# Kernel tuning notes

Hardware: AMD Instinct MI355X
Metric: run time of the kernel (lower is better)

The kernel has to match this reference:

```python
import jax, jax.numpy as jnp
import numpy as np

NEG_INF = -9e15
ALPHA = 0.2  # LeakyReLU negative slope

N = 8192
D_IN = 512
D_OUT = 256


def setup_inputs() -> dict:
    key = jax.random.key(0)
    k1, k2, k3, k4, k5 = jax.random.split(key, 5)
    features = jax.random.normal(k1, (N, D_IN), dtype=jnp.float32)
    adjacency_matrix = jax.random.randint(k2, (N, N), 0, 2, dtype=jnp.int32)
    # learned params (torch Linear stores [out, in]; we use [in, out] layout)
    s_phi = 1.0 / np.sqrt(D_IN)
    W_phi = jax.random.uniform(k3, (D_IN, D_OUT), jnp.float32, -s_phi, s_phi)
    s_v = 1.0 / np.sqrt(D_OUT)
    w_mu = jax.random.uniform(k4, (D_OUT,), jnp.float32, -s_v, s_v)
    w_xi = jax.random.uniform(k5, (D_OUT,), jnp.float32, -s_v, s_v)
    return {"features": features, "adjacency_matrix": adjacency_matrix,
            "W_phi": W_phi, "w_mu": w_mu, "w_xi": w_xi}


def reference(features, adjacency_matrix, W_phi, w_mu, w_xi):
    h = features @ W_phi                                   # [N, d_out]
    mu = h @ w_mu                                          # [N]
    xi = h @ w_xi                                          # [N]
    e = mu[:, None] + xi[None, :]                          # [N, N] additive scores
    e = jnp.where(e >= 0, e, ALPHA * e)                    # LeakyReLU
    e = jnp.where(adjacency_matrix > 0, e, NEG_INF)        # mask non-edges
    a = jax.nn.softmax(e, axis=1)                          # row softmax (dropout p=0)
    out = a @ h                                            # weighted aggregation
    return jax.nn.elu(out)
```

## Files before the change

kernel.cpp:

```cpp
#include <hip/hip_runtime.h>
#include <cstdint>
#include <cstddef>


#define LOG2E 1.44269504f

typedef __attribute__((ext_vector_type(8))) short short8;
typedef __attribute__((ext_vector_type(4))) float floatx4;

using uint_as1 = __attribute__((address_space(1))) unsigned int;
using uint_as3 = __attribute__((address_space(3))) unsigned int;

__device__ __forceinline__ void gld_lds16(const void* g, void* l) {
  __builtin_amdgcn_global_load_lds((const uint_as1*)g, (uint_as3*)l, 16, 0, 0);
}

__device__ __forceinline__ unsigned short f2b(float f) {
  unsigned u = __float_as_uint(f);
  u += 0x7fffu + ((u >> 16) & 1u);
  return (unsigned short)(u >> 16);
}
__device__ __forceinline__ float b2f(short s) {
  return __uint_as_float(((unsigned)(unsigned short)s) << 16);
}

__device__ __forceinline__ unsigned cvtpk_bf16(float a, float b) {
  unsigned r;
  asm("v_cvt_pk_bf16_f32 %0, %1, %2" : "=v"(r) : "v"(a), "v"(b));
  return r;
}

__global__ void k_bitmaskz(const int* __restrict__ adj,
                           const float* __restrict__ Emu, const float* __restrict__ Fmu,
                           const float* __restrict__ Exi, const float* __restrict__ Fxi,
                           unsigned long long* __restrict__ bm, float* __restrict__ zbuf) {
  int gw = (blockIdx.x * 256 + threadIdx.x) >> 6;
  int lane = threadIdx.x & 63;
  float EM = Emu[gw], FM = Fmu[gw];
  size_t w0 = (size_t)gw * 128;
  float z = 0.f;
  for (int r = 0; r < 128; r += 4) {
    size_t wd = w0 + r;
    int v0 = adj[(wd + 0) * 64 + lane];
    int v1 = adj[(wd + 1) * 64 + lane];
    int v2 = adj[(wd + 2) * 64 + lane];
    int v3 = adj[(wd + 3) * 64 + lane];
    float e0 = Exi[(r + 0) * 64 + lane], f0 = Fxi[(r + 0) * 64 + lane];
    float e1 = Exi[(r + 1) * 64 + lane], f1 = Fxi[(r + 1) * 64 + lane];
    float e2 = Exi[(r + 2) * 64 + lane], f2 = Fxi[(r + 2) * 64 + lane];
    float e3 = Exi[(r + 3) * 64 + lane], f3 = Fxi[(r + 3) * 64 + lane];
    unsigned long long m0 = __ballot(v0 != 0);
    unsigned long long m1 = __ballot(v1 != 0);
    unsigned long long m2 = __ballot(v2 != 0);
    unsigned long long m3 = __ballot(v3 != 0);
    z += (v0 != 0) ? fmaxf(EM * e0, FM * f0) : 0.f;
    z += (v1 != 0) ? fmaxf(EM * e1, FM * f1) : 0.f;
    z += (v2 != 0) ? fmaxf(EM * e2, FM * f2) : 0.f;
    z += (v3 != 0) ? fmaxf(EM * e3, FM * f3) : 0.f;
    if (lane == 0) {
      bm[wd] = m0; bm[wd + 1] = m1; bm[wd + 2] = m2; bm[wd + 3] = m3;
    }
  }
#pragma unroll
  for (int off = 32; off > 0; off >>= 1) z += __shfl_xor(z, off);
  if (lane == 0) zbuf[gw] = z;
}

__global__ void k_cvt_features(const float* __restrict__ f, unsigned short* __restrict__ fb) {
  int tid = blockIdx.x * 256 + threadIdx.x;
  float4 v = ((const float4*)f)[tid];
  ushort4 o = {f2b(v.x), f2b(v.y), f2b(v.z), f2b(v.w)};
  *(ushort4*)&fb[tid * 4] = o;
}

__global__ void k_prep_wt(const float* __restrict__ w, unsigned short* __restrict__ wt) {
  int tid = blockIdx.x * 256 + threadIdx.x;
  int n = tid >> 9, k = tid & 511;
  wt[n * 512 + k] = f2b(w[k * 256 + n]);
}

__global__ void k_prep_p(const float* __restrict__ w, const float* __restrict__ wmu,
                         const float* __restrict__ wxi, float* __restrict__ pmu,
                         float* __restrict__ pxi) {
  int tid = blockIdx.x * 256 + threadIdx.x;
  int k = tid >> 2, seg = tid & 3;
  float sm = 0.f, sx = 0.f;
  int base = k * 256 + seg * 64;
#pragma unroll
  for (int c = 0; c < 64; c += 4) {
    float4 wv = *(const float4*)&w[base + c];
    float4 mv = *(const float4*)&wmu[seg * 64 + c];
    float4 xv = *(const float4*)&wxi[seg * 64 + c];
    sm += wv.x * mv.x + wv.y * mv.y + wv.z * mv.z + wv.w * mv.w;
    sx += wv.x * xv.x + wv.y * xv.y + wv.z * xv.z + wv.w * xv.w;
  }
  sm += __shfl_xor(sm, 1); sm += __shfl_xor(sm, 2);
  sx += __shfl_xor(sx, 1); sx += __shfl_xor(sx, 2);
  if (seg == 0) { pmu[k] = sm; pxi[k] = sx; }
}

__global__ void k_mu_xi(const unsigned short* __restrict__ fb, const float* __restrict__ pmu,
                        const float* __restrict__ pxi, float* __restrict__ Emu,
                        float* __restrict__ Fmu, float* __restrict__ Exi,
                        float* __restrict__ Fxi) {
  int w = threadIdx.x >> 6, l = threadIdx.x & 63;
  int i = blockIdx.x * 4 + w;
  short8 fv = *(const short8*)&fb[i * 512 + l * 8];
  float m = 0.f, x = 0.f;
#pragma unroll
  for (int c = 0; c < 8; ++c) {
    float fvf = b2f(fv[c]);
    m = fmaf(fvf, pmu[l * 8 + c], m);
    x = fmaf(fvf, pxi[l * 8 + c], x);
  }
#pragma unroll
  for (int off = 32; off > 0; off >>= 1) {
    m += __shfl_xor(m, off);
    x += __shfl_xor(x, off);
  }
  if (l == 0) {
    float ms = m * LOG2E, xs = x * LOG2E;
    Emu[i] = __builtin_amdgcn_exp2f(ms);
    Fmu[i] = __builtin_amdgcn_exp2f(0.2f * ms);
    Exi[i] = __builtin_amdgcn_exp2f(xs);
    Fxi[i] = __builtin_amdgcn_exp2f(0.2f * xs);
  }
}

__global__ __launch_bounds__(256, 2) void k_gemm1(const unsigned short* __restrict__ fb,
                                                  const unsigned short* __restrict__ wt,
                                                  unsigned short* __restrict__ ht) {
  __shared__ __align__(16) unsigned short As[64 * 64];
  __shared__ __align__(16) unsigned short Bs[128 * 64];
  int t = threadIdx.x, w = t >> 6, l = t & 63;
  int bm_ = blockIdx.x >> 1, bn = blockIdx.x & 1;
  int m0 = bm_ * 64, n0 = bn * 128;
  int lr = l >> 3, lg = l & 7, g = lg ^ lr;
  int kg = l >> 4, ln = l & 15;
  floatx4 zero = {0.f, 0.f, 0.f, 0.f};
  floatx4 acc[4][2];
#pragma unroll
  for (int mf = 0; mf < 4; ++mf)
#pragma unroll
    for (int nf = 0; nf < 2; ++nf) acc[mf][nf] = zero;

  for (int it = 0; it < 8; ++it) {
    int k0 = it * 64;
#pragma unroll
    for (int q = 0; q < 2; ++q) {
      int row = w * 16 + q * 8 + lr;
      const void* gp = fb + (size_t)(m0 + row) * 512 + k0 + g * 8;
      int lb = __builtin_amdgcn_readfirstlane((w * 16 + q * 8) * 64);
      gld_lds16(gp, &As[lb]);
    }
#pragma unroll
    for (int q = 0; q < 4; ++q) {
      int row = w * 32 + q * 8 + lr;
      const void* gp = wt + (size_t)(n0 + row) * 512 + k0 + g * 8;
      int lb = __builtin_amdgcn_readfirstlane((w * 32 + q * 8) * 64);
      gld_lds16(gp, &Bs[lb]);
    }
    __syncthreads();
#pragma unroll
    for (int ks = 0; ks < 2; ++ks) {
      int gg = ks * 4 + kg;
      int swz = (gg ^ (ln & 7)) * 8;
      short8 bfr[2];
#pragma unroll
      for (int nf = 0; nf < 2; ++nf)
        bfr[nf] = *(const short8*)&Bs[(w * 32 + nf * 16 + ln) * 64 + swz];
#pragma unroll
      for (int mf = 0; mf < 4; ++mf) {
        short8 afr = *(const short8*)&As[(mf * 16 + ln) * 64 + swz];
#pragma unroll
        for (int nf = 0; nf < 2; ++nf)
          acc[mf][nf] = __builtin_amdgcn_mfma_f32_16x16x32_bf16(afr, bfr[nf], acc[mf][nf], 0, 0, 0);
      }
    }
    __syncthreads();
  }
#pragma unroll
  for (int mf = 0; mf < 4; ++mf)
#pragma unroll
    for (int nf = 0; nf < 2; ++nf) {
      int ng = n0 + w * 32 + nf * 16 + ln;
      int mg = m0 + mf * 16 + kg * 4;
      ushort4 o = {f2b(acc[mf][nf][0]), f2b(acc[mf][nf][1]),
                   f2b(acc[mf][nf][2]), f2b(acc[mf][nf][3])};
      *(ushort4*)&ht[(size_t)ng * 8192 + mg] = o;
    }
}

__global__ __launch_bounds__(512, 2) void k_gatt8(const unsigned char* __restrict__ bm8,
                                                  const unsigned short* __restrict__ ht,
                                                  const float* __restrict__ Emu,
                                                  const float* __restrict__ Fmu,
                                                  const float* __restrict__ Exi,
                                                  const float* __restrict__ Fxi,
                                                  float* __restrict__ nump) {
  __shared__ __align__(16) unsigned short Bs[2][256 * 128];
  __shared__ __align__(16) float EfE[1024];
  __shared__ __align__(16) float EfF[1024];

  int t = threadIdx.x, w = t >> 6, l = t & 63;
  int ln = l & 15, kg = l >> 4;
  int jb = blockIdx.x & 7, ig = blockIdx.x >> 3;
  int i0 = ig * 256;
  int jc0 = jb * 1024;

  if (t < 256) {
    *(float4*)&EfE[t * 4] = *(const float4*)&Exi[jc0 + t * 4];
  } else {
    int t2 = t - 256;
    *(float4*)&EfF[t2 * 4] = *(const float4*)&Fxi[jc0 + t2 * 4];
  }

  float EM[2], FM[2];
  const uint4* bprow[2];
#pragma unroll
  for (int mf = 0; mf < 2; ++mf) {
    int i = i0 + w * 32 + mf * 16 + ln;
    EM[mf] = Emu[i];
    FM[mf] = Fmu[i];
    bprow[mf] = (const uint4*)(bm8 + (size_t)i * 1024 + jb * 128);
  }

  floatx4 zero = {0.f, 0.f, 0.f, 0.f};
  floatx4 acc[2][16];
#pragma unroll
  for (int mf = 0; mf < 2; ++mf)
#pragma unroll
    for (int nf = 0; nf < 16; ++nf) acc[mf][nf] = zero;

#define STAGE(win_, b_)                                                       \
  {                                                                           \
    int j0_ = jc0 + (win_) * 128;                                             \
    _Pragma("unroll")                                                         \
    for (int q = 0; q < 8; ++q) {                                             \
      int r0 = w * 32 + q * 4;                                                \
      int row = r0 + (l >> 4);                                                \
      int g = (l & 15) ^ (row & 15);                                          \
      const void* gp = ht + (size_t)row * 8192 + j0_ + g * 8;                 \
      int lb = __builtin_amdgcn_readfirstlane((b_) * (256 * 128) + r0 * 128); \
      gld_lds16(gp, &Bs[0][lb]);                                              \
    }                                                                         \
  }

  uint4 bc[2], bnx[2];
#pragma unroll
  for (int mf = 0; mf < 2; ++mf) bc[mf] = bprow[mf][0];
  STAGE(0, 0);
  __syncthreads();

  for (int win = 0; win < 8; ++win) {
    int buf = win & 1;
    if (win < 7) {
      STAGE(win + 1, buf ^ 1);
#pragma unroll
      for (int mf = 0; mf < 2; ++mf) bnx[mf] = bprow[mf][win + 1];
    }
#pragma unroll
    for (int ksl = 0; ksl < 4; ++ksl) {
      int gran = ksl * 4 + kg;
      int jl = win * 128 + gran * 8;
      float4 e0 = *(const float4*)&EfE[jl];
      float4 e1 = *(const float4*)&EfE[jl + 4];
      float4 f0 = *(const float4*)&EfF[jl];
      float4 f1 = *(const float4*)&EfF[jl + 4];
      float ex[8] = {e0.x, e0.y, e0.z, e0.w, e1.x, e1.y, e1.z, e1.w};
      float fx[8] = {f0.x, f0.y, f0.z, f0.w, f1.x, f1.y, f1.z, f1.w};
      short8 af[2];
#pragma unroll
      for (int mf = 0; mf < 2; ++mf) {
        unsigned word = (ksl == 0) ? bc[mf].x : (ksl == 1) ? bc[mf].y
                      : (ksl == 2) ? bc[mf].z : bc[mf].w;
        unsigned bits = (word >> (kg * 8)) & 0xffu;
        float A = EM[mf], F = FM[mf];
        union { unsigned u[4]; short8 s; } cv;
#pragma unroll
        for (int p = 0; p < 4; ++p) {
          float m0 = fmaxf(A * ex[2 * p], F * fx[2 * p]);
          float m1 = fmaxf(A * ex[2 * p + 1], F * fx[2 * p + 1]);
          m0 = (bits & (1u << (2 * p))) ? m0 : 0.f;
          m1 = (bits & (1u << (2 * p + 1))) ? m1 : 0.f;
          cv.u[p] = cvtpk_bf16(m0, m1);
        }
        af[mf] = cv.s;
      }
#pragma unroll
      for (int half = 0; half < 2; ++half) {
        short8 bfv[8];
#pragma unroll
        for (int nf = 0; nf < 8; ++nf) {
          int n = half * 128 + nf * 16 + ln;
          bfv[nf] = *(const short8*)&Bs[buf][n * 128 + ((gran ^ (n & 15)) * 8)];
        }
#pragma unroll
        for (int mf = 0; mf < 2; ++mf)
#pragma unroll
          for (int nf = 0; nf < 8; ++nf)
            acc[mf][half * 8 + nf] = __builtin_amdgcn_mfma_f32_16x16x32_bf16(
                af[mf], bfv[nf], acc[mf][half * 8 + nf], 0, 0, 0);
      }
    }
    __syncthreads();
#pragma unroll
    for (int mf = 0; mf < 2; ++mf) bc[mf] = bnx[mf];
  }
#undef STAGE

  float* np = nump + (size_t)jb * (8192 * 256);
#pragma unroll
  for (int mf = 0; mf < 2; ++mf) {
    int rowb = i0 + w * 32 + mf * 16 + kg * 4;
#pragma unroll
    for (int r = 0; r < 4; ++r) {
      float* rp = np + (size_t)(rowb + r) * 256;
#pragma unroll
      for (int nf = 0; nf < 16; ++nf)
        rp[nf * 16 + ln] = acc[mf][nf][r];
    }
  }
}

__global__ void k_final(const float* __restrict__ nump, const float* __restrict__ zbuf,
                        float* __restrict__ out) {
  int tid = blockIdx.x * 256 + threadIdx.x;
  int i = tid >> 6;
  float zi = 1.0f / zbuf[i];
  float4 v = {0.f, 0.f, 0.f, 0.f};
#pragma unroll
  for (int p = 0; p < 8; ++p) {
    float4 s = *(const float4*)&nump[(size_t)p * (8192 * 256) + tid * 4];
    v.x += s.x; v.y += s.y; v.z += s.z; v.w += s.w;
  }
  v.x *= zi; v.y *= zi; v.z *= zi; v.w *= zi;
  v.x = (v.x > 0.f) ? v.x : (__builtin_amdgcn_exp2f(v.x * LOG2E) - 1.f);
  v.y = (v.y > 0.f) ? v.y : (__builtin_amdgcn_exp2f(v.y * LOG2E) - 1.f);
  v.z = (v.z > 0.f) ? v.z : (__builtin_amdgcn_exp2f(v.z * LOG2E) - 1.f);
  v.w = (v.w > 0.f) ? v.w : (__builtin_amdgcn_exp2f(v.w * LOG2E) - 1.f);
  *(float4*)&out[tid * 4] = v;
}

extern "C" void kernel_launch(void* const* d_in, const int* in_sizes, int n_in,
                              void* d_out, int out_size, void* d_ws, size_t ws_size,
                              hipStream_t stream) {
  const float* features = (const float*)d_in[0];
  const int* adjm = (const int*)d_in[1];
  const float* W_phi = (const float*)d_in[2];
  const float* w_mu = (const float*)d_in[3];
  const float* w_xi = (const float*)d_in[4];
  float* out = (float*)d_out;

  char* ws = (char*)d_ws;
  unsigned short* fb  = (unsigned short*)(ws + 0);
  unsigned short* ht  = (unsigned short*)(ws + 8388608);
  unsigned short* wt  = (unsigned short*)(ws + 12582912);
  float* pmu = (float*)(ws + 12845056);
  float* pxi = (float*)(ws + 12847104);
  float* Emu = (float*)(ws + 12849152);
  float* Fmu = (float*)(ws + 12881920);
  float* Exi = (float*)(ws + 12914688);
  float* Fxi = (float*)(ws + 12947456);
  float* zbuf = (float*)(ws + 12980224);
  unsigned char* bmask = (unsigned char*)(ws + 13631488);
  float* nump = (float*)(ws + 25165824);

  k_cvt_features<<<4096, 256, 0, stream>>>(features, fb);
  k_prep_wt<<<512, 256, 0, stream>>>(W_phi, wt);
  k_prep_p<<<8, 256, 0, stream>>>(W_phi, w_mu, w_xi, pmu, pxi);
  k_mu_xi<<<2048, 256, 0, stream>>>(fb, pmu, pxi, Emu, Fmu, Exi, Fxi);
  k_gemm1<<<256, 256, 0, stream>>>(fb, wt, ht);
  k_bitmaskz<<<2048, 256, 0, stream>>>(adjm, Emu, Fmu, Exi, Fxi,
                                       (unsigned long long*)bmask, zbuf);
  k_gatt8<<<256, 512, 0, stream>>>(bmask, ht, Emu, Fmu, Exi, Fxi, nump);
  k_final<<<2048, 256, 0, stream>>>(nump, zbuf, out);
}
```

Before: 467.8 us.

## Fuse adjacency masking and softmax denominator into attention GEMM kernel

Removes the separate bitmask/denominator kernel. The attention kernel now streams the int32 adjacency tile into LDS with async global-to-LDS loads alongside the bf16 h tile, masks scores directly, and accumulates partial row sums per column block. The final kernel sums the eight partial denominators. This skips writing and re-reading an intermediate bitmask and the extra launch, but the K window shrinks from 128 to 32 per stage. That means four times as many barriers, and the main kernel now reads the full 256MB int adjacency itself.

```diff
diff --git a/kernel.cpp b/kernel.cpp
--- a/kernel.cpp
+++ b/kernel.cpp
@@ -28,42 +28,6 @@
   unsigned r;
   asm("v_cvt_pk_bf16_f32 %0, %1, %2" : "=v"(r) : "v"(a), "v"(b));
   return r;
-}
-
-__global__ void k_bitmaskz(const int* __restrict__ adj,
-                           const float* __restrict__ Emu, const float* __restrict__ Fmu,
-                           const float* __restrict__ Exi, const float* __restrict__ Fxi,
-                           unsigned long long* __restrict__ bm, float* __restrict__ zbuf) {
-  int gw = (blockIdx.x * 256 + threadIdx.x) >> 6;
-  int lane = threadIdx.x & 63;
-  float EM = Emu[gw], FM = Fmu[gw];
-  size_t w0 = (size_t)gw * 128;
-  float z = 0.f;
-  for (int r = 0; r < 128; r += 4) {
-    size_t wd = w0 + r;
-    int v0 = adj[(wd + 0) * 64 + lane];
-    int v1 = adj[(wd + 1) * 64 + lane];
-    int v2 = adj[(wd + 2) * 64 + lane];
-    int v3 = adj[(wd + 3) * 64 + lane];
-    float e0 = Exi[(r + 0) * 64 + lane], f0 = Fxi[(r + 0) * 64 + lane];
-    float e1 = Exi[(r + 1) * 64 + lane], f1 = Fxi[(r + 1) * 64 + lane];
-    float e2 = Exi[(r + 2) * 64 + lane], f2 = Fxi[(r + 2) * 64 + lane];
-    float e3 = Exi[(r + 3) * 64 + lane], f3 = Fxi[(r + 3) * 64 + lane];
-    unsigned long long m0 = __ballot(v0 != 0);
-    unsigned long long m1 = __ballot(v1 != 0);
-    unsigned long long m2 = __ballot(v2 != 0);
-    unsigned long long m3 = __ballot(v3 != 0);
-    z += (v0 != 0) ? fmaxf(EM * e0, FM * f0) : 0.f;
-    z += (v1 != 0) ? fmaxf(EM * e1, FM * f1) : 0.f;
-    z += (v2 != 0) ? fmaxf(EM * e2, FM * f2) : 0.f;
-    z += (v3 != 0) ? fmaxf(EM * e3, FM * f3) : 0.f;
-    if (lane == 0) {
-      bm[wd] = m0; bm[wd + 1] = m1; bm[wd + 2] = m2; bm[wd + 3] = m3;
-    }
-  }
-#pragma unroll
-  for (int off = 32; off > 0; off >>= 1) z += __shfl_xor(z, off);
-  if (lane == 0) zbuf[gw] = z;
 }
 
 __global__ void k_cvt_features(const float* __restrict__ f, unsigned short* __restrict__ fb) {
@@ -191,14 +155,16 @@
     }
 }
 
-__global__ __launch_bounds__(512, 2) void k_gatt8(const unsigned char* __restrict__ bm8,
+__global__ __launch_bounds__(512, 2) void k_gatt9(const int* __restrict__ adjm,
                                                   const unsigned short* __restrict__ ht,
                                                   const float* __restrict__ Emu,
                                                   const float* __restrict__ Fmu,
                                                   const float* __restrict__ Exi,
                                                   const float* __restrict__ Fxi,
-                                                  float* __restrict__ nump) {
-  __shared__ __align__(16) unsigned short Bs[2][256 * 128];
+                                                  float* __restrict__ nump,
+                                                  float* __restrict__ zpart) {
+  __shared__ __align__(16) unsigned short Bs[2][256 * 32];
+  __shared__ __align__(16) int Aj[2][256 * 32];
   __shared__ __align__(16) float EfE[1024];
   __shared__ __align__(16) float EfF[1024];
 
@@ -216,13 +182,11 @@
   }
 
   float EM[2], FM[2];
-  const uint4* bprow[2];
 #pragma unroll
   for (int mf = 0; mf < 2; ++mf) {
     int i = i0 + w * 32 + mf * 16 + ln;
     EM[mf] = Emu[i];
     FM[mf] = Fmu[i];
-    bprow[mf] = (const uint4*)(bm8 + (size_t)i * 1024 + jb * 128);
   }
 
   floatx4 zero = {0.f, 0.f, 0.f, 0.f};
@@ -231,83 +195,106 @@
   for (int mf = 0; mf < 2; ++mf)
 #pragma unroll
     for (int nf = 0; nf < 16; ++nf) acc[mf][nf] = zero;
-
-#define STAGE(win_, b_)                                                       \
-  {                                                                           \
-    int j0_ = jc0 + (win_) * 128;                                             \
-    _Pragma("unroll")                                                         \
-    for (int q = 0; q < 8; ++q) {                                             \
-      int r0 = w * 32 + q * 4;                                                \
-      int row = r0 + (l >> 4);                                                \
-      int g = (l & 15) ^ (row & 15);                                          \
-      const void* gp = ht + (size_t)row * 8192 + j0_ + g * 8;                 \
-      int lb = __builtin_amdgcn_readfirstlane((b_) * (256 * 128) + r0 * 128); \
-      gld_lds16(gp, &Bs[0][lb]);                                              \
-    }                                                                         \
-  }
-
-  uint4 bc[2], bnx[2];
-#pragma unroll
-  for (int mf = 0; mf < 2; ++mf) bc[mf] = bprow[mf][0];
-  STAGE(0, 0);
+  float zacc[2] = {0.f, 0.f};
+
+#define STAGE_B(win_, b_)                                                   \
+  {                                                                         \
+    int j0_ = jc0 + (win_) * 32;                                            \
+    _Pragma("unroll")                                                       \
+    for (int q = 0; q < 2; ++q) {                                           \
+      int rowbase = w * 32 + q * 16;                                        \
+      int row = rowbase + (l >> 2);                                         \
+      int g = (l & 3) ^ ((row >> 1) & 3);                                   \
+      const void* gp = ht + (size_t)row * 8192 + j0_ + g * 8;               \
+      int lb = __builtin_amdgcn_readfirstlane((b_) * (256 * 32) + rowbase * 32); \
+      gld_lds16(gp, &((unsigned short*)Bs)[lb]);                            \
+    }                                                                       \
+  }
+
+#define STAGE_A(win_, b_)                                                   \
+  {                                                                         \
+    int j0_ = jc0 + (win_) * 32;                                            \
+    _Pragma("unroll")                                                       \
+    for (int q = 0; q < 4; ++q) {                                           \
+      int rowbase = w * 32 + q * 8;                                         \
+      int rr = l >> 3;                                                      \
+      int row = rowbase + rr;                                               \
+      int wslot = (l & 7) ^ rr;                                             \
+      const void* gp = adjm + (size_t)(i0 + row) * 8192 + j0_ + wslot * 4;  \
+      int lb = __builtin_amdgcn_readfirstlane((b_) * (256 * 32) + rowbase * 32); \
+      gld_lds16(gp, &((int*)Aj)[lb]);                                       \
+    }                                                                       \
+  }
+
+  STAGE_B(0, 0);
+  STAGE_A(0, 0);
   __syncthreads();
 
-  for (int win = 0; win < 8; ++win) {
+  for (int win = 0; win < 32; ++win) {
     int buf = win & 1;
-    if (win < 7) {
-      STAGE(win + 1, buf ^ 1);
-#pragma unroll
-      for (int mf = 0; mf < 2; ++mf) bnx[mf] = bprow[mf][win + 1];
-    }
-#pragma unroll
-    for (int ksl = 0; ksl < 4; ++ksl) {
-      int gran = ksl * 4 + kg;
-      int jl = win * 128 + gran * 8;
-      float4 e0 = *(const float4*)&EfE[jl];
-      float4 e1 = *(const float4*)&EfE[jl + 4];
-      float4 f0 = *(const float4*)&EfF[jl];
-      float4 f1 = *(const float4*)&EfF[jl + 4];
-      float ex[8] = {e0.x, e0.y, e0.z, e0.w, e1.x, e1.y, e1.z, e1.w};
-      float fx[8] = {f0.x, f0.y, f0.z, f0.w, f1.x, f1.y, f1.z, f1.w};
-      short8 af[2];
-#pragma unroll
-      for (int mf = 0; mf < 2; ++mf) {
-        unsigned word = (ksl == 0) ? bc[mf].x : (ksl == 1) ? bc[mf].y
-                      : (ksl == 2) ? bc[mf].z : bc[mf].w;
-        unsigned bits = (word >> (kg * 8)) & 0xffu;
-        float A = EM[mf], F = FM[mf];
-        union { unsigned u[4]; short8 s; } cv;
-#pragma unroll
-        for (int p = 0; p < 4; ++p) {
-          float m0 = fmaxf(A * ex[2 * p], F * fx[2 * p]);
-          float m1 = fmaxf(A * ex[2 * p + 1], F * fx[2 * p + 1]);
-          m0 = (bits & (1u << (2 * p))) ? m0 : 0.f;
-          m1 = (bits & (1u << (2 * p + 1))) ? m1 : 0.f;
-          cv.u[p] = cvtpk_bf16(m0, m1);
-        }
-        af[mf] = cv.s;
+    if (win < 31) {
+      STAGE_B(win + 1, buf ^ 1);
+      STAGE_A(win + 1, buf ^ 1);
+    }
+    int jl = win * 32 + kg * 8;
+    float4 e0 = *(const float4*)&EfE[jl];
+    float4 e1 = *(const float4*)&EfE[jl + 4];
+    float4 f0 = *(const float4*)&EfF[jl];
+    float4 f1 = *(const float4*)&EfF[jl + 4];
+    float ex[8] = {e0.x, e0.y, e0.z, e0.w, e1.x, e1.y, e1.z, e1.w};
+    float fx[8] = {f0.x, f0.y, f0.z, f0.w, f1.x, f1.y, f1.z, f1.w};
+    short8 af[2];
+#pragma unroll
+    for (int mf = 0; mf < 2; ++mf) {
+      int i_loc = w * 32 + mf * 16 + ln;
+      int rr = ln & 7;
+      const int* arow = &((const int*)Aj)[buf * (256 * 32) + i_loc * 32];
+      int4 a0 = *(const int4*)&arow[((2 * kg) ^ rr) * 4];
+      int4 a1 = *(const int4*)&arow[((2 * kg + 1) ^ rr) * 4];
+      int av[8] = {a0.x, a0.y, a0.z, a0.w, a1.x, a1.y, a1.z, a1.w};
+      float A = EM[mf], F = FM[mf];
+      union { unsigned u[4]; short8 s; } cv;
+      float zs = 0.f;
+#pragma unroll
+      for (int p = 0; p < 4; ++p) {
+        float m0 = fmaxf(A * ex[2 * p], F * fx[2 * p]);
+        float m1 = fmaxf(A * ex[2 * p + 1], F * fx[2 * p + 1]);
+        m0 = (av[2 * p] != 0) ? m0 : 0.f;
+        m1 = (av[2 * p + 1] != 0) ? m1 : 0.f;
+        zs += m0;
+        zs += m1;
+        cv.u[p] = cvtpk_bf16(m0, m1);
       }
-#pragma unroll
-      for (int half = 0; half < 2; ++half) {
-        short8 bfv[8];
-#pragma unroll
-        for (int nf = 0; nf < 8; ++nf) {
-          int n = half * 128 + nf * 16 + ln;
-          bfv[nf] = *(const short8*)&Bs[buf][n * 128 + ((gran ^ (n & 15)) * 8)];
-        }
-#pragma unroll
-        for (int mf = 0; mf < 2; ++mf)
-#pragma unroll
-          for (int nf = 0; nf < 8; ++nf)
-            acc[mf][half * 8 + nf] = __builtin_amdgcn_mfma_f32_16x16x32_bf16(
-                af[mf], bfv[nf], acc[mf][half * 8 + nf], 0, 0, 0);
+      zacc[mf] += zs;
+      af[mf] = cv.s;
+    }
+#pragma unroll
+    for (int half = 0; half < 2; ++half) {
+      short8 bfv[8];
+#pragma unroll
+      for (int nf = 0; nf < 8; ++nf) {
+        int n = half * 128 + nf * 16 + ln;
+        bfv[nf] = *(const short8*)&Bs[buf][n * 32 + ((kg ^ ((n >> 1) & 3)) * 8)];
       }
+#pragma unroll
+      for (int mf = 0; mf < 2; ++mf)
+#pragma unroll
+        for (int nf = 0; nf < 8; ++nf)
+          acc[mf][half * 8 + nf] = __builtin_amdgcn_mfma_f32_16x16x32_bf16(
+              af[mf], bfv[nf], acc[mf][half * 8 + nf], 0, 0, 0);
     }
     __syncthreads();
-#pragma unroll
-    for (int mf = 0; mf < 2; ++mf) bc[mf] = bnx[mf];
-  }
-#undef STAGE
+  }
+#undef STAGE_B
+#undef STAGE_A
+
+#pragma unroll
+  for (int mf = 0; mf < 2; ++mf) {
+    float z = zacc[mf];
+    z += __shfl_xor(z, 16);
+    z += __shfl_xor(z, 32);
+    if (l < 16) zpart[(size_t)jb * 8192 + i0 + w * 32 + mf * 16 + ln] = z;
+  }
 
   float* np = nump + (size_t)jb * (8192 * 256);
 #pragma unroll
@@ -323,11 +310,14 @@
   }
 }
 
-__global__ void k_final(const float* __restrict__ nump, const float* __restrict__ zbuf,
+__global__ void k_final(const float* __restrict__ nump, const float* __restrict__ zpart,
                         float* __restrict__ out) {
   int tid = blockIdx.x * 256 + threadIdx.x;
   int i = tid >> 6;
-  float zi = 1.0f / zbuf[i];
+  float z = 0.f;
+#pragma unroll
+  for (int p = 0; p < 8; ++p) z += zpart[(size_t)p * 8192 + i];
+  float zi = 1.0f / z;
   float4 v = {0.f, 0.f, 0.f, 0.f};
 #pragma unroll
   for (int p = 0; p < 8; ++p) {
@@ -362,8 +352,7 @@
   float* Fmu = (float*)(ws + 12881920);
   float* Exi = (float*)(ws + 12914688);
   float* Fxi = (float*)(ws + 12947456);
-  float* zbuf = (float*)(ws + 12980224);
-  unsigned char* bmask = (unsigned char*)(ws + 13631488);
+  float* zpart = (float*)(ws + 12980224);
   float* nump = (float*)(ws + 25165824);
 
   k_cvt_features<<<4096, 256, 0, stream>>>(features, fb);
@@ -371,8 +360,6 @@
   k_prep_p<<<8, 256, 0, stream>>>(W_phi, w_mu, w_xi, pmu, pxi);
   k_mu_xi<<<2048, 256, 0, stream>>>(fb, pmu, pxi, Emu, Fmu, Exi, Fxi);
   k_gemm1<<<256, 256, 0, stream>>>(fb, wt, ht);
-  k_bitmaskz<<<2048, 256, 0, stream>>>(adjm, Emu, Fmu, Exi, Fxi,
-                                       (unsigned long long*)bmask, zbuf);
-  k_gatt8<<<256, 512, 0, stream>>>(bmask, ht, Emu, Fmu, Exi, Fxi, nump);
-  k_final<<<2048, 256, 0, stream>>>(nump, zbuf, out);
-}
+  k_gatt9<<<256, 512, 0, stream>>>(adjm, ht, Emu, Fmu, Exi, Fxi, nump, zpart);
+  k_final<<<2048, 256, 0, stream>>>(nump, zpart, out);
+}
```

Measured after the change: 449.0 us. 1.04x faster.
